# Kernel optimization log

Hardware: AMD Instinct MI355X
Metric: run time of the kernel (lower is better)

The kernel has to match this reference:

```python
import jax, jax.numpy as jnp
import numpy as np

B, L, C, D, K = 32, 36864, 16, 512, 24


def setup_inputs() -> dict:
    key = jax.random.key(0)
    ks = jax.random.split(key, 5)
    x = jax.random.normal(ks[0], (B, L, C), jnp.float32)
    # offset-conv weights scaled small so predicted offsets are O(0.2) (kaiming-ish but tame)
    w_off = jax.random.normal(ks[1], (2 * K, C, K), jnp.float32) * 0.01
    b_off = jax.random.normal(ks[2], (2 * K,), jnp.float32) * 0.05
    w_def = jax.random.normal(ks[3], (D, C, K), jnp.float32) * (2.0 / (C * K)) ** 0.5
    b_def = jax.random.normal(ks[4], (D,), jnp.float32) * 0.05
    return {"x": x, "w_off": w_off, "b_off": b_off, "w_def": w_def, "b_def": b_def}


def reference(x, w_off, b_off, w_def, b_def):
    # x: [B, L, C] -> torch view [B, C, 1, L]; H == 1 throughout.
    Bn, Ln, Cn = x.shape
    twoK, _, Kn = w_off.shape
    Lout = Ln // Kn
    xc = jnp.transpose(x, (0, 2, 1))                 # [B, C, L]
    xk = xc.reshape(Bn, Cn, Lout, Kn)                # stride == kernel -> non-overlapping windows
    # offset conv: [B, 2K, Lout]
    off = jnp.einsum('bclk,ock->bol', xk, w_off) + b_off[None, :, None]
    off = off.reshape(Bn, Kn, 2, Lout)               # channel 2k -> dy, 2k+1 -> dx (torchvision layout)
    dy = jnp.transpose(off[:, :, 0, :], (0, 2, 1))   # [B, Lout, K]
    dx = jnp.transpose(off[:, :, 1, :], (0, 2, 1))   # [B, Lout, K]
    # sampling positions along width; base = w_out*K + k
    base = jnp.arange(Lout * Kn, dtype=x.dtype).reshape(Lout, Kn)
    px = base[None] + dx                             # [B, Lout, K]
    # height bilinear weight: with H=1, contribution at h=0 is max(0, 1-|dy|)
    wy = jnp.maximum(jnp.array(0, x.dtype), 1.0 - jnp.abs(dy))
    # width bilinear with zero padding (torchvision bilinear_interpolate semantics)
    valid = (px > -1.0) & (px < Ln)
    x0 = jnp.floor(px)
    lw = px - x0                                     # weight for right neighbor
    i0 = x0.astype(jnp.int32)
    i1 = i0 + 1
    m0 = (valid & (i0 >= 0) & (i0 < Ln)).astype(x.dtype)
    m1 = (valid & (i1 >= 0) & (i1 < Ln)).astype(x.dtype)
    i0c = jnp.broadcast_to(jnp.clip(i0, 0, Ln - 1).reshape(Bn, 1, Lout * Kn), (Bn, Cn, Lout * Kn))
    i1c = jnp.broadcast_to(jnp.clip(i1, 0, Ln - 1).reshape(Bn, 1, Lout * Kn), (Bn, Cn, Lout * Kn))
    v0 = jnp.take_along_axis(xc, i0c, axis=2).reshape(Bn, Cn, Lout, Kn)
    v1 = jnp.take_along_axis(xc, i1c, axis=2).reshape(Bn, Cn, Lout, Kn)
    val = (v0 * ((1.0 - lw) * m0)[:, None] + v1 * (lw * m1)[:, None]) * wy[:, None]  # [B,C,Lout,K]
    out = jnp.einsum('bclk,dck->bld', val, w_def) + b_def  # [B, Lout, D]
    return out
```

## Files before the change

kernel.cpp:

```cpp
#include <hip/hip_runtime.h>
#include <stdint.h>

#define BATCH 32
#define LLEN  36864
#define CCH   16
#define DOUT  512
#define KW    24
#define LOUT  1536
#define MROWS (BATCH * LOUT)
#define CK    384
#define TWOK  48

typedef float fx4 __attribute__((ext_vector_type(4)));
typedef float f32x4 __attribute__((ext_vector_type(4)));
typedef __bf16 bf16x8 __attribute__((ext_vector_type(8)));

__global__ __launch_bounds__(256) void prep_kernel(
    const float* __restrict__ w_off, const float* __restrict__ w_def,
    float* __restrict__ woff_t, __bf16* __restrict__ wdef_t)
{
    int idx = blockIdx.x * 256 + threadIdx.x;
    if (idx < TWOK * CK) {
        int o = idx / CK, rem = idx % CK;
        int k = rem >> 4, c = rem & 15;
        woff_t[idx] = w_off[o * CK + c * KW + k];
    }
    if (idx < DOUT * CK) {
        int d = idx / CK, rem = idx % CK;
        int k = rem >> 4, c = rem & 15;
        wdef_t[idx] = (__bf16)w_def[d * CK + c * KW + k];
    }
}

#define WB 128
#define KC 64
#define WS 68

__global__ __launch_bounds__(256) void off_samp_kernel(
    const float* __restrict__ x, const float* __restrict__ woff_t,
    const float* __restrict__ b_off, __bf16* __restrict__ val)
{
    __shared__ char smem[61952];
    float* winS  = (float*)smem;
    float* woffS = (float*)(smem + 34816);
    float* offS  = (float*)smem;
    int*   i0S   = (int*)(smem + 25088);
    float* w0S   = (float*)(smem + 37376);
    float* w1S   = (float*)(smem + 49664);

    const int t  = threadIdx.x;
    const int m0 = blockIdx.x * WB;
    const int wg = t & 31;
    const int o0 = (t >> 5) * 6;

    float acc[4][6];
#pragma unroll
    for (int u = 0; u < 4; ++u)
#pragma unroll
        for (int v = 0; v < 6; ++v) acc[u][v] = 0.f;

    for (int kt = 0; kt < CK; kt += KC) {
        __syncthreads();
#pragma unroll
        for (int i = 0; i < 8; ++i) {
            int q = t + 256 * i;
            int row = q >> 4, c4 = q & 15;
            *(fx4*)&winS[row * WS + c4 * 4] =
                *(const fx4*)&x[(size_t)(m0 + row) * CK + kt + c4 * 4];
        }
#pragma unroll
        for (int i = 0; i < 3; ++i) {
            int q = t + 256 * i;
            int row = q >> 4, c4 = q & 15;
            *(fx4*)&woffS[row * WS + c4 * 4] =
                *(const fx4*)&woff_t[row * CK + kt + c4 * 4];
        }
        __syncthreads();
        for (int jj = 0; jj < KC; jj += 4) {
            fx4 wv[4], of[6];
#pragma unroll
            for (int u = 0; u < 4; ++u)
                wv[u] = *(const fx4*)&winS[(wg + 32 * u) * WS + jj];
#pragma unroll
            for (int v = 0; v < 6; ++v)
                of[v] = *(const fx4*)&woffS[(o0 + v) * WS + jj];
#pragma unroll
            for (int u = 0; u < 4; ++u)
#pragma unroll
                for (int v = 0; v < 6; ++v)
                    acc[u][v] += wv[u].x * of[v].x + wv[u].y * of[v].y +
                                 wv[u].z * of[v].z + wv[u].w * of[v].w;
        }
    }
    __syncthreads();
    float boffv[6];
#pragma unroll
    for (int v = 0; v < 6; ++v) boffv[v] = b_off[o0 + v];
#pragma unroll
    for (int u = 0; u < 4; ++u)
#pragma unroll
        for (int v = 0; v < 6; ++v)
            offS[(wg + 32 * u) * 49 + o0 + v] = acc[u][v] + boffv[v];
    __syncthreads();

    const int b     = m0 / LOUT;
    const int lbase = m0 % LOUT;
#pragma unroll
    for (int i = 0; i < 12; ++i) {
        int q = t + 256 * i;
        int k = q >> 7, w = q & 127;
        float dy = offS[w * 49 + 2 * k];
        float dx = offS[w * 49 + 2 * k + 1];
        float wy = fmaxf(0.f, 1.f - fabsf(dy));
        float px = (float)((lbase + w) * KW + k) + dx;
        float x0f = floorf(px);
        float lw = px - x0f;
        int  i0 = (int)x0f;
        bool valid = (px > -1.0f) && (px < (float)LLEN);
        float w0v = (valid && i0 >= 0)          ? (1.f - lw) * wy : 0.f;
        float w1v = (valid && (i0 + 1) < LLEN)  ? lw * wy         : 0.f;
        int i0c = min(max(i0, 0), LLEN - 1);
        int i1c = min(max(i0 + 1, 0), LLEN - 1);
        i0S[k * 128 + w] = (int)((unsigned)i0c | ((unsigned)i1c << 16));
        w0S[k * 128 + w] = w0v;
        w1S[k * 128 + w] = w1v;
    }
    __syncthreads();

    const float* xb = x + (size_t)b * LLEN * CCH;
    __bf16* valb = val + (size_t)m0 * CK;
#pragma unroll 2
    for (int ww = 0; ww < 64; ++ww) {
        int base = ww * 768;
#pragma unroll
        for (int s = 0; s < 3; ++s) {
            int p = t + s * 256;
            int hi = (p >= CK) ? 1 : 0;
            int w2 = ww * 2 + hi;
            int j  = p - hi * CK;
            int k = j >> 4, c = j & 15;
            unsigned pk = (unsigned)i0S[k * 128 + w2];
            int i0c = (int)(pk & 0xffffu);
            int i1c = (int)(pk >> 16);
            float v = w0S[k * 128 + w2] * xb[i0c * CCH + c] +
                      w1S[k * 128 + w2] * xb[i1c * CCH + c];
            valb[base + p] = (__bf16)v;
        }
    }
}

#define BM 128
#define BN 128
#define BK 64

__device__ __forceinline__ void gload16(void* lds, const void* g)
{
    __builtin_amdgcn_global_load_lds(
        (const __attribute__((address_space(1))) uint32_t*)g,
        (__attribute__((address_space(3))) uint32_t*)lds, 16, 0, 0);
}

__global__ __launch_bounds__(256) void gemm_kernel(
    const __bf16* __restrict__ Aval, const __bf16* __restrict__ Bw,
    const float* __restrict__ bias, float* __restrict__ out)
{
    __shared__ __bf16 As[BM * BK];
    __shared__ __bf16 Bs[BN * BK];

    const int t = threadIdx.x;
    const int m0 = blockIdx.x * BM;
    const int n0 = blockIdx.y * BN;
    const int wave = t >> 6, lane = t & 63;
    const int wr = wave >> 1, wc = wave & 1;
    const int quad = lane >> 4, l16 = lane & 15;

    f32x4 acc[4][4];
#pragma unroll
    for (int i = 0; i < 4; ++i)
#pragma unroll
        for (int j = 0; j < 4; ++j) acc[i][j] = (f32x4){0.f, 0.f, 0.f, 0.f};

    const __bf16* Ag = Aval + (size_t)m0 * CK;
    const __bf16* Bg = Bw + (size_t)n0 * CK;

    for (int kt = 0; kt < CK; kt += BK) {
        __syncthreads();
#pragma unroll
        for (int it = 0; it < 4; ++it) {
            int q = it * 256 + t;
            int r = q >> 3, c8 = q & 7;
            gload16(&As[q * 8], Ag + (size_t)r * CK + kt + c8 * 8);
            gload16(&Bs[q * 8], Bg + (size_t)r * CK + kt + c8 * 8);
        }
        __syncthreads();
#pragma unroll
        for (int ks = 0; ks < 2; ++ks) {
            bf16x8 af[4], bfr[4];
#pragma unroll
            for (int i = 0; i < 4; ++i) {
                int row = wr * 64 + i * 16 + l16;
                af[i] = *(const bf16x8*)&As[row * BK + ks * 32 + quad * 8];
                int col = wc * 64 + i * 16 + l16;
                bfr[i] = *(const bf16x8*)&Bs[col * BK + ks * 32 + quad * 8];
            }
#pragma unroll
            for (int i = 0; i < 4; ++i)
#pragma unroll
                for (int j = 0; j < 4; ++j)
                    acc[i][j] = __builtin_amdgcn_mfma_f32_16x16x32_bf16(
                        af[i], bfr[j], acc[i][j], 0, 0, 0);
        }
    }

#pragma unroll
    for (int i = 0; i < 4; ++i) {
#pragma unroll
        for (int j = 0; j < 4; ++j) {
            int col = n0 + wc * 64 + j * 16 + l16;
            float bj = bias[col];
#pragma unroll
            for (int r = 0; r < 4; ++r) {
                int row = m0 + wr * 64 + i * 16 + quad * 4 + r;
                out[(size_t)row * DOUT + col] = acc[i][j][r] + bj;
            }
        }
    }
}

extern "C" void kernel_launch(void* const* d_in, const int* in_sizes, int n_in,
                              void* d_out, int out_size, void* d_ws, size_t ws_size,
                              hipStream_t stream)
{
    const float* x     = (const float*)d_in[0];
    const float* w_off = (const float*)d_in[1];
    const float* b_off = (const float*)d_in[2];
    const float* w_def = (const float*)d_in[3];
    const float* b_def = (const float*)d_in[4];
    float* out = (float*)d_out;

    char* ws = (char*)d_ws;
    __bf16* val    = (__bf16*)ws;
    __bf16* wdef_t = (__bf16*)(ws + 37748736);
    float*  woff_t = (float*)(ws + 38141952);

    prep_kernel<<<768, 256, 0, stream>>>(w_off, w_def, woff_t, wdef_t);
    off_samp_kernel<<<MROWS / WB, 256, 0, stream>>>(x, woff_t, b_off, val);
    gemm_kernel<<<dim3(MROWS / BM, DOUT / BN), 256, 0, stream>>>(val, wdef_t, b_def, out);
}
```

Baseline: 234.6 us.

## Split offset conv onto MFMA, separate vectorized gather, widen swizzled GEMM tiles

The fused offset/sampling kernel is split in two. An offsets kernel computes the offset conv with bf16 MFMA and writes packed bf16 dy/dx pairs. A gather kernel then handles one (row, k) sample per thread and does vectorized 16-channel bilinear loads and stores. The GEMM moves to 128x256 tiles with 512 threads and an XOR-swizzled LDS layout to reduce bank conflicts. Offsets are now computed in bf16, which loses precision in the sampling positions, and the extra dxy buffer adds a global round trip.

```diff
diff --git a/kernel.cpp b/kernel.cpp
--- a/kernel.cpp
+++ b/kernel.cpp
@@ -10,158 +10,151 @@
 #define MROWS (BATCH * LOUT)
 #define CK    384
 #define TWOK  48
+#define NMK   (MROWS * KW)
 
 typedef float fx4 __attribute__((ext_vector_type(4)));
 typedef float f32x4 __attribute__((ext_vector_type(4)));
 typedef __bf16 bf16x8 __attribute__((ext_vector_type(8)));
+typedef uint32_t u32x4 __attribute__((ext_vector_type(4)));
+
+__device__ __forceinline__ void gload16(void* lds, const void* g)
+{
+    __builtin_amdgcn_global_load_lds(
+        (const __attribute__((address_space(1))) uint32_t*)g,
+        (__attribute__((address_space(3))) uint32_t*)lds, 16, 0, 0);
+}
 
 __global__ __launch_bounds__(256) void prep_kernel(
     const float* __restrict__ w_off, const float* __restrict__ w_def,
-    float* __restrict__ woff_t, __bf16* __restrict__ wdef_t)
+    __bf16* __restrict__ woff_b, __bf16* __restrict__ wdef_b)
 {
     int idx = blockIdx.x * 256 + threadIdx.x;
     if (idx < TWOK * CK) {
         int o = idx / CK, rem = idx % CK;
         int k = rem >> 4, c = rem & 15;
-        woff_t[idx] = w_off[o * CK + c * KW + k];
+        woff_b[idx] = (__bf16)w_off[o * CK + c * KW + k];
     }
     if (idx < DOUT * CK) {
         int d = idx / CK, rem = idx % CK;
         int k = rem >> 4, c = rem & 15;
-        wdef_t[idx] = (__bf16)w_def[d * CK + c * KW + k];
-    }
-}
-
-#define WB 128
-#define KC 64
-#define WS 68
-
-__global__ __launch_bounds__(256) void off_samp_kernel(
-    const float* __restrict__ x, const float* __restrict__ woff_t,
-    const float* __restrict__ b_off, __bf16* __restrict__ val)
-{
-    __shared__ char smem[61952];
-    float* winS  = (float*)smem;
-    float* woffS = (float*)(smem + 34816);
-    float* offS  = (float*)smem;
-    int*   i0S   = (int*)(smem + 25088);
-    float* w0S   = (float*)(smem + 37376);
-    float* w1S   = (float*)(smem + 49664);
-
-    const int t  = threadIdx.x;
-    const int m0 = blockIdx.x * WB;
-    const int wg = t & 31;
-    const int o0 = (t >> 5) * 6;
-
-    float acc[4][6];
-#pragma unroll
-    for (int u = 0; u < 4; ++u)
-#pragma unroll
-        for (int v = 0; v < 6; ++v) acc[u][v] = 0.f;
-
-    for (int kt = 0; kt < CK; kt += KC) {
-        __syncthreads();
-#pragma unroll
-        for (int i = 0; i < 8; ++i) {
-            int q = t + 256 * i;
-            int row = q >> 4, c4 = q & 15;
-            *(fx4*)&winS[row * WS + c4 * 4] =
-                *(const fx4*)&x[(size_t)(m0 + row) * CK + kt + c4 * 4];
-        }
-#pragma unroll
-        for (int i = 0; i < 3; ++i) {
-            int q = t + 256 * i;
-            int row = q >> 4, c4 = q & 15;
-            *(fx4*)&woffS[row * WS + c4 * 4] =
-                *(const fx4*)&woff_t[row * CK + kt + c4 * 4];
-        }
-        __syncthreads();
-        for (int jj = 0; jj < KC; jj += 4) {
-            fx4 wv[4], of[6];
-#pragma unroll
-            for (int u = 0; u < 4; ++u)
-                wv[u] = *(const fx4*)&winS[(wg + 32 * u) * WS + jj];
-#pragma unroll
-            for (int v = 0; v < 6; ++v)
-                of[v] = *(const fx4*)&woffS[(o0 + v) * WS + jj];
-#pragma unroll
-            for (int u = 0; u < 4; ++u)
-#pragma unroll
-                for (int v = 0; v < 6; ++v)
-                    acc[u][v] += wv[u].x * of[v].x + wv[u].y * of[v].y +
-                                 wv[u].z * of[v].z + wv[u].w * of[v].w;
-        }
+        wdef_b[idx] = (__bf16)w_def[d * CK + c * KW + k];
+    }
+}
+
+__global__ __launch_bounds__(256, 3) void offsets_kernel(
+    const float* __restrict__ x, const __bf16* __restrict__ woff_b,
+    const float* __restrict__ b_off, uint32_t* __restrict__ dxy)
+{
+    __shared__ __bf16 Bs[TWOK * 392];
+    __shared__ float  offS[64 * 49];
+
+    const int t = threadIdx.x;
+#pragma unroll
+    for (int i = 0; i < 9; ++i) {
+        int ch = t + 256 * i;
+        int row = ch / 48, cc = ch % 48;
+        *(u32x4*)&Bs[row * 392 + cc * 8] =
+            *(const u32x4*)&woff_b[row * CK + cc * 8];
     }
     __syncthreads();
-    float boffv[6];
-#pragma unroll
-    for (int v = 0; v < 6; ++v) boffv[v] = b_off[o0 + v];
-#pragma unroll
-    for (int u = 0; u < 4; ++u)
-#pragma unroll
-        for (int v = 0; v < 6; ++v)
-            offS[(wg + 32 * u) * 49 + o0 + v] = acc[u][v] + boffv[v];
+
+    const int wave = t >> 6, lane = t & 63;
+    const int quad = lane >> 4, l16 = lane & 15;
+    const int m0 = blockIdx.x * 64;
+    const int row = m0 + wave * 16 + l16;
+    const float* xr = x + (size_t)row * CK;
+
+    f32x4 acc[3] = {};
+#pragma unroll
+    for (int ks = 0; ks < 12; ++ks) {
+        int k0 = ks * 32 + quad * 8;
+        fx4 a0 = *(const fx4*)&xr[k0];
+        fx4 a1 = *(const fx4*)&xr[k0 + 4];
+        bf16x8 af;
+        af[0] = (__bf16)a0.x; af[1] = (__bf16)a0.y;
+        af[2] = (__bf16)a0.z; af[3] = (__bf16)a0.w;
+        af[4] = (__bf16)a1.x; af[5] = (__bf16)a1.y;
+        af[6] = (__bf16)a1.z; af[7] = (__bf16)a1.w;
+#pragma unroll
+        for (int j = 0; j < 3; ++j) {
+            bf16x8 bf = *(const bf16x8*)&Bs[(j * 16 + l16) * 392 + k0];
+            acc[j] = __builtin_amdgcn_mfma_f32_16x16x32_bf16(af, bf, acc[j], 0, 0, 0);
+        }
+    }
+#pragma unroll
+    for (int j = 0; j < 3; ++j)
+#pragma unroll
+        for (int r = 0; r < 4; ++r)
+            offS[(wave * 16 + quad * 4 + r) * 49 + j * 16 + l16] = acc[j][r];
     __syncthreads();
 
-    const int b     = m0 / LOUT;
-    const int lbase = m0 % LOUT;
-#pragma unroll
-    for (int i = 0; i < 12; ++i) {
-        int q = t + 256 * i;
-        int k = q >> 7, w = q & 127;
-        float dy = offS[w * 49 + 2 * k];
-        float dx = offS[w * 49 + 2 * k + 1];
-        float wy = fmaxf(0.f, 1.f - fabsf(dy));
-        float px = (float)((lbase + w) * KW + k) + dx;
-        float x0f = floorf(px);
-        float lw = px - x0f;
-        int  i0 = (int)x0f;
-        bool valid = (px > -1.0f) && (px < (float)LLEN);
-        float w0v = (valid && i0 >= 0)          ? (1.f - lw) * wy : 0.f;
-        float w1v = (valid && (i0 + 1) < LLEN)  ? lw * wy         : 0.f;
-        int i0c = min(max(i0, 0), LLEN - 1);
-        int i1c = min(max(i0 + 1, 0), LLEN - 1);
-        i0S[k * 128 + w] = (int)((unsigned)i0c | ((unsigned)i1c << 16));
-        w0S[k * 128 + w] = w0v;
-        w1S[k * 128 + w] = w1v;
-    }
-    __syncthreads();
+#pragma unroll
+    for (int s = 0; s < 6; ++s) {
+        int id = t + 256 * s;
+        int r = id / 24, k = id - r * 24;
+        float dy = offS[r * 49 + 2 * k]     + b_off[2 * k];
+        float dx = offS[r * 49 + 2 * k + 1] + b_off[2 * k + 1];
+        union { __bf16 h[2]; uint32_t u; } p;
+        p.h[0] = (__bf16)dy; p.h[1] = (__bf16)dx;
+        dxy[(size_t)m0 * KW + id] = p.u;
+    }
+}
+
+__global__ __launch_bounds__(256) void gather_kernel(
+    const float* __restrict__ x, const uint32_t* __restrict__ dxy,
+    __bf16* __restrict__ val)
+{
+    int id = blockIdx.x * 256 + threadIdx.x;
+    int b = id / (LOUT * KW);
+    int pos = id - b * (LOUT * KW);
+
+    union { uint32_t u; __bf16 h[2]; } p;
+    p.u = dxy[id];
+    float dy = (float)p.h[0], dx = (float)p.h[1];
+
+    float wy  = fmaxf(0.f, 1.f - fabsf(dy));
+    float px  = (float)pos + dx;
+    float x0f = floorf(px);
+    float lw  = px - x0f;
+    int   i0  = (int)x0f;
+    bool valid = (px > -1.0f) && (px < (float)LLEN);
+    float w0 = (valid && i0 >= 0)         ? (1.f - lw) * wy : 0.f;
+    float w1 = (valid && (i0 + 1) < LLEN) ? lw * wy         : 0.f;
+    int i0c = min(max(i0, 0), LLEN - 1);
+    int i1c = min(max(i0 + 1, 0), LLEN - 1);
 
     const float* xb = x + (size_t)b * LLEN * CCH;
-    __bf16* valb = val + (size_t)m0 * CK;
-#pragma unroll 2
-    for (int ww = 0; ww < 64; ++ww) {
-        int base = ww * 768;
-#pragma unroll
-        for (int s = 0; s < 3; ++s) {
-            int p = t + s * 256;
-            int hi = (p >= CK) ? 1 : 0;
-            int w2 = ww * 2 + hi;
-            int j  = p - hi * CK;
-            int k = j >> 4, c = j & 15;
-            unsigned pk = (unsigned)i0S[k * 128 + w2];
-            int i0c = (int)(pk & 0xffffu);
-            int i1c = (int)(pk >> 16);
-            float v = w0S[k * 128 + w2] * xb[i0c * CCH + c] +
-                      w1S[k * 128 + w2] * xb[i1c * CCH + c];
-            valb[base + p] = (__bf16)v;
-        }
-    }
+    const fx4* p0 = (const fx4*)&xb[(size_t)i0c * CCH];
+    const fx4* p1 = (const fx4*)&xb[(size_t)i1c * CCH];
+
+    bf16x8 o0, o1;
+#pragma unroll
+    for (int q = 0; q < 2; ++q) {
+        fx4 v0 = p0[q], v1 = p1[q];
+        o0[q * 4 + 0] = (__bf16)(w0 * v0.x + w1 * v1.x);
+        o0[q * 4 + 1] = (__bf16)(w0 * v0.y + w1 * v1.y);
+        o0[q * 4 + 2] = (__bf16)(w0 * v0.z + w1 * v1.z);
+        o0[q * 4 + 3] = (__bf16)(w0 * v0.w + w1 * v1.w);
+    }
+#pragma unroll
+    for (int q = 0; q < 2; ++q) {
+        fx4 v0 = p0[q + 2], v1 = p1[q + 2];
+        o1[q * 4 + 0] = (__bf16)(w0 * v0.x + w1 * v1.x);
+        o1[q * 4 + 1] = (__bf16)(w0 * v0.y + w1 * v1.y);
+        o1[q * 4 + 2] = (__bf16)(w0 * v0.z + w1 * v1.z);
+        o1[q * 4 + 3] = (__bf16)(w0 * v0.w + w1 * v1.w);
+    }
+    __bf16* vp = val + (size_t)id * 16;
+    *(bf16x8*)vp       = o0;
+    *(bf16x8*)(vp + 8) = o1;
 }
 
 #define BM 128
-#define BN 128
+#define BN 256
 #define BK 64
 
-__device__ __forceinline__ void gload16(void* lds, const void* g)
-{
-    __builtin_amdgcn_global_load_lds(
-        (const __attribute__((address_space(1))) uint32_t*)g,
-        (__attribute__((address_space(3))) uint32_t*)lds, 16, 0, 0);
-}
-
-__global__ __launch_bounds__(256) void gemm_kernel(
-    const __bf16* __restrict__ Aval, const __bf16* __restrict__ Bw,
+__global__ __launch_bounds__(512, 4) void gemm_kernel(
+    const __bf16* __restrict__ A, const __bf16* __restrict__ Bw,
     const float* __restrict__ bias, float* __restrict__ out)
 {
     __shared__ __bf16 As[BM * BK];
@@ -171,26 +164,28 @@
     const int m0 = blockIdx.x * BM;
     const int n0 = blockIdx.y * BN;
     const int wave = t >> 6, lane = t & 63;
-    const int wr = wave >> 1, wc = wave & 1;
     const int quad = lane >> 4, l16 = lane & 15;
-
-    f32x4 acc[4][4];
-#pragma unroll
-    for (int i = 0; i < 4; ++i)
-#pragma unroll
-        for (int j = 0; j < 4; ++j) acc[i][j] = (f32x4){0.f, 0.f, 0.f, 0.f};
-
-    const __bf16* Ag = Aval + (size_t)m0 * CK;
+    const int wr = wave >> 2, wc = wave & 3;
+
+    f32x4 acc[4][4] = {};
+    const __bf16* Ag = A + (size_t)m0 * CK;
     const __bf16* Bg = Bw + (size_t)n0 * CK;
 
     for (int kt = 0; kt < CK; kt += BK) {
         __syncthreads();
 #pragma unroll
+        for (int it = 0; it < 2; ++it) {
+            int q = it * 512 + t;
+            int r = q >> 3, c8 = q & 7;
+            int sc = c8 ^ (r & 7);
+            gload16(&As[q * 8], Ag + (size_t)r * CK + kt + sc * 8);
+        }
+#pragma unroll
         for (int it = 0; it < 4; ++it) {
-            int q = it * 256 + t;
+            int q = it * 512 + t;
             int r = q >> 3, c8 = q & 7;
-            gload16(&As[q * 8], Ag + (size_t)r * CK + kt + c8 * 8);
-            gload16(&Bs[q * 8], Bg + (size_t)r * CK + kt + c8 * 8);
+            int sc = c8 ^ (r & 7);
+            gload16(&Bs[q * 8], Bg + (size_t)r * CK + kt + sc * 8);
         }
         __syncthreads();
 #pragma unroll
@@ -199,9 +194,9 @@
 #pragma unroll
             for (int i = 0; i < 4; ++i) {
                 int row = wr * 64 + i * 16 + l16;
-                af[i] = *(const bf16x8*)&As[row * BK + ks * 32 + quad * 8];
+                af[i] = *(const bf16x8*)&As[row * BK + (((ks * 4 + quad) ^ (row & 7)) * 8)];
                 int col = wc * 64 + i * 16 + l16;
-                bfr[i] = *(const bf16x8*)&Bs[col * BK + ks * 32 + quad * 8];
+                bfr[i] = *(const bf16x8*)&Bs[col * BK + (((ks * 4 + quad) ^ (col & 7)) * 8)];
             }
 #pragma unroll
             for (int i = 0; i < 4; ++i)
@@ -213,16 +208,15 @@
     }
 
 #pragma unroll
-    for (int i = 0; i < 4; ++i) {
-#pragma unroll
-        for (int j = 0; j < 4; ++j) {
-            int col = n0 + wc * 64 + j * 16 + l16;
-            float bj = bias[col];
-#pragma unroll
-            for (int r = 0; r < 4; ++r) {
-                int row = m0 + wr * 64 + i * 16 + quad * 4 + r;
-                out[(size_t)row * DOUT + col] = acc[i][j][r] + bj;
-            }
+    for (int j = 0; j < 4; ++j) {
+        int col = n0 + wc * 64 + j * 16 + l16;
+        float bj = bias[col];
+#pragma unroll
+        for (int i = 0; i < 4; ++i) {
+            int rowb = m0 + wr * 64 + i * 16 + quad * 4;
+#pragma unroll
+            for (int r = 0; r < 4; ++r)
+                out[(size_t)(rowb + r) * DOUT + col] = acc[i][j][r] + bj;
         }
     }
 }
@@ -239,11 +233,13 @@
     float* out = (float*)d_out;
 
     char* ws = (char*)d_ws;
-    __bf16* val    = (__bf16*)ws;
-    __bf16* wdef_t = (__bf16*)(ws + 37748736);
-    float*  woff_t = (float*)(ws + 38141952);
-
-    prep_kernel<<<768, 256, 0, stream>>>(w_off, w_def, woff_t, wdef_t);
-    off_samp_kernel<<<MROWS / WB, 256, 0, stream>>>(x, woff_t, b_off, val);
-    gemm_kernel<<<dim3(MROWS / BM, DOUT / BN), 256, 0, stream>>>(val, wdef_t, b_def, out);
-}
+    __bf16*   val    = (__bf16*)ws;
+    __bf16*   wdef_b = (__bf16*)(ws + 37748736);
+    __bf16*   woff_b = (__bf16*)(ws + 38141952);
+    uint32_t* dxy    = (uint32_t*)(ws + 38178816);
+
+    prep_kernel<<<768, 256, 0, stream>>>(w_off, w_def, woff_b, wdef_b);
+    offsets_kernel<<<MROWS / 64, 256, 0, stream>>>(x, woff_b, b_off, dxy);
+    gather_kernel<<<NMK / 256, 256, 0, stream>>>(x, dxy, val);
+    gemm_kernel<<<dim3(MROWS / BM, DOUT / BN), 512, 0, stream>>>(val, wdef_b, b_def, out);
+}
```

After: 226.2 us. -3.6%, faster.
